# Optimization experiments

Measured on AMD Instinct MI355X. Metric: run time of the kernel, lower is better.

## Reference

```python
import jax, jax.numpy as jnp
import numpy as np

N_EMBD = 2048
N_HEAD = 32
N_GROUPS = 8
HEAD_DIM = N_EMBD // N_HEAD
Q_PER_KV = N_HEAD // N_GROUPS
QKV_DIM = (Q_PER_KV + 2) * N_GROUPS * HEAD_DIM


def apply_rope(x, cos, sin):
    # x: [B, nH, T, hd]; cos/sin: [T, rot//2]
    B, nH, T, hd = x.shape
    rot = min(sin.shape[1] * 2, hd)
    half = rot // 2
    x_rot, x_pass = x[..., :rot], x[..., rot:]
    c = cos[:T, :half][None, None]  # [1,1,T,half]
    s = sin[:T, :half][None, None]
    x1, x2 = x_rot[..., :half], x_rot[..., half:]
    x1_ = x1 * c - x2 * s
    x2_ = x2 * c + x1 * s
    return jnp.concatenate([x1_, x2_, x_pass], axis=-1)


def setup_inputs() -> dict:
    key = jax.random.key(0)
    k1, k2, k3, k4, k5 = jax.random.split(key, 5)
    B, T = 2, 2048
    x = jax.random.normal(k1, (B, T, N_EMBD), dtype=jnp.float32)
    cos = jax.random.uniform(k2, (T, HEAD_DIM // 2), dtype=jnp.float32)
    sin = jax.random.uniform(k3, (T, HEAD_DIM // 2), dtype=jnp.float32)
    attn_w = jax.random.normal(k4, (QKV_DIM, N_EMBD), dtype=jnp.float32) * (1.0 / np.sqrt(N_EMBD))
    proj_w = jax.random.normal(k5, (N_EMBD, N_EMBD), dtype=jnp.float32) * (1.0 / np.sqrt(N_EMBD))
    return {"x": x, "cos": cos, "sin": sin, "attn_w": attn_w, "proj_w": proj_w}


def reference(x, cos, sin, attn_w, proj_w):
    B, T, E = x.shape
    qkv = jnp.einsum('bte,fe->btf', x, attn_w)  # [B,T,QKV_DIM]
    qkv = qkv.reshape(B, T, N_GROUPS, Q_PER_KV + 2, HEAD_DIM)
    q = qkv[:, :, :, :Q_PER_KV].reshape(B, T, N_HEAD, HEAD_DIM)
    k = qkv[:, :, :, Q_PER_KV]      # [B,T,G,hd]
    v = qkv[:, :, :, Q_PER_KV + 1]  # [B,T,G,hd]
    # [B, heads, T, hd] layout; GQA repeat_interleave of K/V to full head count
    q = q.transpose(0, 2, 1, 3)
    k = jnp.repeat(k.transpose(0, 2, 1, 3), Q_PER_KV, axis=1)
    v = jnp.repeat(v.transpose(0, 2, 1, 3), Q_PER_KV, axis=1)
    q = apply_rope(q, cos, sin)
    k = apply_rope(k, cos, sin)
    scale = 1.0 / np.sqrt(HEAD_DIM)
    att = jax.nn.softmax(jnp.einsum('bhqd,bhkd->bhqk', q, k) * scale, axis=-1)
    out = jnp.einsum('bhqk,bhkd->bhqd', att, v)  # [B,nH,T,hd]
    out = out.transpose(0, 2, 1, 3).reshape(B, T, N_HEAD * HEAD_DIM)
    return jnp.einsum('bte,fe->btf', out, proj_w)
```

## Files before the change

### kernel.cpp

```cpp
#include <hip/hip_runtime.h>

typedef unsigned short u16;
typedef unsigned int u32;
typedef __bf16 bf16x8 __attribute__((ext_vector_type(8)));
typedef float f32x4 __attribute__((ext_vector_type(4)));
typedef float f32x16 __attribute__((ext_vector_type(16)));
typedef unsigned int u32x4 __attribute__((ext_vector_type(4)));

__device__ __forceinline__ u16 f2bf(float f) {
    u32 u = __builtin_bit_cast(u32, f);
    u32 r = u + 0x7FFFu + ((u >> 16) & 1u);
    return (u16)(r >> 16);
}
__device__ __forceinline__ u32 pack_bf16(float v0, float v1) {
    u32 a = __builtin_bit_cast(u32, v0) + 0x8000u;
    u32 b = __builtin_bit_cast(u32, v1) + 0x8000u;
    return __builtin_amdgcn_perm(b, a, 0x07060302u);
}
__device__ __forceinline__ u32 cvtpk(float lo, float hi) {
    u32 r;
    asm("v_cvt_pk_bf16_f32 %0, %1, %2" : "=v"(r) : "v"(lo), "v"(hi));
    return r;
}
__device__ __forceinline__ void plswap(u32& a, u32& b) {
    asm("v_permlane32_swap_b32 %0, %1" : "+v"(a), "+v"(b));
}
__device__ __forceinline__ void gload16(const u16* g, u16* l) {
    __builtin_amdgcn_global_load_lds(
        (const __attribute__((address_space(1))) u32*)g,
        (__attribute__((address_space(3))) u32*)l, 16, 0, 0);
}

#define QSCALE 0.18033688011111793f

__global__ __launch_bounds__(256) void cvt_kernel(const float* __restrict__ in,
                                                  u16* __restrict__ out, int n4) {
    int i = blockIdx.x * 256 + threadIdx.x;
    if (i >= n4) return;
    float4 f = reinterpret_cast<const float4*>(in)[i];
    u32 lo = (u32)f2bf(f.x) | ((u32)f2bf(f.y) << 16);
    u32 hi = (u32)f2bf(f.z) | ((u32)f2bf(f.w) << 16);
    reinterpret_cast<uint2*>(out)[i] = make_uint2(lo, hi);
}

__global__ __launch_bounds__(256) void gemm_qkv(const u16* __restrict__ A,
                                                const u16* __restrict__ Bw,
                                                const float* __restrict__ cosb,
                                                const float* __restrict__ sinb,
                                                u16* __restrict__ Qo,
                                                u16* __restrict__ Ko,
                                                u16* __restrict__ Vt) {
    __shared__ __align__(16) u16 As[2 * 128 * 32];
    __shared__ __align__(16) u16 Bs[2 * 128 * 32];
    const int tid = threadIdx.x;
    const int wave = tid >> 6, lane = tid & 63, quad = lane >> 4, l15 = lane & 15;
    const int wm = wave >> 1, wn = wave & 1;
    const int m0 = blockIdx.x * 128, n0 = blockIdx.y * 128;
    const int K = 2048;
    const int lrow = lane >> 2, lcol = (lane & 3) * 8;
    f32x4 acc[4][4];
#pragma unroll
    for (int a = 0; a < 4; a++)
#pragma unroll
        for (int b = 0; b < 4; b++) acc[a][b] = (f32x4){0.f, 0.f, 0.f, 0.f};
    for (int kk = 0; kk < K; kk += 64) {
        __syncthreads();
#pragma unroll
        for (int p = 0; p < 2; p++)
#pragma unroll
            for (int c = 0; c < 2; c++) {
                const int rA = wave * 32 + c * 16;
                gload16(A  + (size_t)(m0 + rA + lrow) * K + kk + p * 32 + lcol,
                        &As[p * 4096 + rA * 32]);
                gload16(Bw + (size_t)(n0 + rA + lrow) * K + kk + p * 32 + lcol,
                        &Bs[p * 4096 + rA * 32]);
            }
        __syncthreads();
#pragma unroll
        for (int p = 0; p < 2; p++) {
            bf16x8 af[4], bfr[4];
#pragma unroll
            for (int t = 0; t < 4; t++) {
                af[t]  = *reinterpret_cast<const bf16x8*>(
                    &As[p * 4096 + (wm * 64 + t * 16 + l15) * 32 + quad * 8]);
                bfr[t] = *reinterpret_cast<const bf16x8*>(
                    &Bs[p * 4096 + (wn * 64 + t * 16 + l15) * 32 + quad * 8]);
            }
#pragma unroll
            for (int tm = 0; tm < 4; tm++)
#pragma unroll
                for (int tn = 0; tn < 4; tn++)
                    acc[tm][tn] = __builtin_amdgcn_mfma_f32_16x16x32_bf16(af[tm], bfr[tn], acc[tm][tn], 0, 0, 0);
        }
    }
    const int slot_base = n0 + wn * 64;
    const int G = slot_base / 384;
    const int slot = (slot_base % 384) / 64;
    const int bb = m0 >> 11;
    const int tb0 = (m0 & 2047) + wm * 64 + quad * 4;
    if (slot == 5) {
        u16* vbase = Vt + ((size_t)(bb * 8 + G) * 64) * 2048;
#pragma unroll
        for (int tm = 0; tm < 4; tm++) {
            const int trow = tb0 + tm * 16;
#pragma unroll
            for (int tn = 0; tn < 4; tn++) {
                const int d = tn * 16 + l15;
                uint2 pk;
                pk.x = pack_bf16(acc[tm][tn][0], acc[tm][tn][1]);
                pk.y = pack_bf16(acc[tm][tn][2], acc[tm][tn][3]);
                *reinterpret_cast<uint2*>(vbase + (size_t)d * 2048 + trow) = pk;
            }
        }
    } else {
        const float sc = (slot < 4) ? QSCALE : 1.0f;
        u16* obase = (slot < 4)
            ? Qo + ((size_t)(bb * 32 + G * 4 + slot) * 2048) * 64
            : Ko + ((size_t)(bb * 8 + G) * 2048) * 64;
#pragma unroll
        for (int tm = 0; tm < 4; tm++) {
#pragma unroll
            for (int i = 0; i < 4; i++) {
                const int t = tb0 + tm * 16 + i;
#pragma unroll
                for (int tn = 0; tn < 2; tn++) {
                    const int dh = tn * 16 + l15;
                    float c = cosb[t * 32 + dh], s = sinb[t * 32 + dh];
                    float x1 = acc[tm][tn][i], x2 = acc[tm][tn + 2][i];
                    obase[(size_t)t * 64 + dh]      = f2bf((x1 * c - x2 * s) * sc);
                    obase[(size_t)t * 64 + dh + 32] = f2bf((x2 * c + x1 * s) * sc);
                }
            }
        }
    }
}

__global__ __launch_bounds__(256) void gemm_bt(const u16* __restrict__ A,
                                               const u16* __restrict__ Bw,
                                               float* __restrict__ Cf,
                                               int M, int N, int K) {
    __shared__ __align__(16) u16 As[2 * 128 * 32];
    __shared__ __align__(16) u16 Bs[2 * 128 * 32];
    const int tid = threadIdx.x;
    const int wave = tid >> 6, lane = tid & 63, quad = lane >> 4, l15 = lane & 15;
    const int wm = wave >> 1, wn = wave & 1;
    const int m0 = blockIdx.x * 128, n0 = blockIdx.y * 128;
    const int lrow = lane >> 2, lcol = (lane & 3) * 8;
    f32x4 acc[4][4];
#pragma unroll
    for (int a = 0; a < 4; a++)
#pragma unroll
        for (int b = 0; b < 4; b++) acc[a][b] = (f32x4){0.f, 0.f, 0.f, 0.f};
    for (int kk = 0; kk < K; kk += 64) {
        __syncthreads();
#pragma unroll
        for (int p = 0; p < 2; p++)
#pragma unroll
            for (int c = 0; c < 2; c++) {
                const int rA = wave * 32 + c * 16;
                gload16(A  + (size_t)(m0 + rA + lrow) * K + kk + p * 32 + lcol,
                        &As[p * 4096 + rA * 32]);
                gload16(Bw + (size_t)(n0 + rA + lrow) * K + kk + p * 32 + lcol,
                        &Bs[p * 4096 + rA * 32]);
            }
        __syncthreads();
#pragma unroll
        for (int p = 0; p < 2; p++) {
            bf16x8 af[4], bfr[4];
#pragma unroll
            for (int t = 0; t < 4; t++) {
                af[t]  = *reinterpret_cast<const bf16x8*>(
                    &As[p * 4096 + (wm * 64 + t * 16 + l15) * 32 + quad * 8]);
                bfr[t] = *reinterpret_cast<const bf16x8*>(
                    &Bs[p * 4096 + (wn * 64 + t * 16 + l15) * 32 + quad * 8]);
            }
#pragma unroll
            for (int tm = 0; tm < 4; tm++)
#pragma unroll
                for (int tn = 0; tn < 4; tn++)
                    acc[tm][tn] = __builtin_amdgcn_mfma_f32_16x16x32_bf16(af[tm], bfr[tn], acc[tm][tn], 0, 0, 0);
        }
    }
#pragma unroll
    for (int tm = 0; tm < 4; tm++) {
        const int r0 = m0 + wm * 64 + tm * 16 + quad * 4;
#pragma unroll
        for (int tn = 0; tn < 4; tn++) {
            const int c = n0 + wn * 64 + tn * 16 + l15;
#pragma unroll
            for (int i = 0; i < 4; i++) Cf[(size_t)(r0 + i) * N + c] = acc[tm][tn][i];
        }
    }
}

__global__ __launch_bounds__(256, 4) void attn(const u16* __restrict__ Q,
                                               const u16* __restrict__ Kg,
                                               const u16* __restrict__ Vt,
                                               u16* __restrict__ O) {
    __shared__ __align__(16) u16 Ks[2 * 64 * 64];
    __shared__ __align__(16) u16 Vts[2 * 64 * 64];
    const int tid = threadIdx.x, w = tid >> 6, lane = tid & 63;
    const int half = lane >> 5, l31 = lane & 31;
    const int rsub = lane >> 3;
    const int csub = (lane & 7) ^ rsub;
    const int swz = (l31 & 7) << 3;
    const int q0 = blockIdx.x * 128;
    const int h = blockIdx.y, b = blockIdx.z, g = h >> 2;
    const u16* qb = Q + (((size_t)(b * 32 + h)) * 2048 + q0) * 64;
    const u16* kb = Kg + ((size_t)(b * 8 + g)) * 2048 * 64;
    const u16* vb = Vt + ((size_t)(b * 8 + g)) * 64 * 2048;

#pragma unroll
    for (int i = 0; i < 4; i++) {
        const int r = w * 32 + i * 8;
        gload16(qb + (size_t)(r + rsub) * 64 + csub * 8, Ks + r * 64);
    }
    __syncthreads();
    bf16x8 qf[4];
#pragma unroll
    for (int ks = 0; ks < 4; ks++)
        qf[ks] = *reinterpret_cast<const bf16x8*>(
            &Ks[(w * 32 + l31) * 64 + ((ks * 16 + half * 8) ^ swz)]);
    __syncthreads();

    f32x16 Oa[2];
#pragma unroll
    for (int t = 0; t < 2; t++)
#pragma unroll
        for (int i = 0; i < 16; i++) Oa[t][i] = 0.f;
    float lsum = 0.f;

    auto stage_kv = [&](int kk, int bsel) {
        u16* kd = Ks + bsel * 4096;
        u16* vd = Vts + bsel * 4096;
        const u16* kg = kb + (size_t)kk * 64;
        const u16* vg = vb + kk;
#pragma unroll
        for (int i = 0; i < 2; i++) {
            const int r = w * 16 + i * 8;
            gload16(kg + (size_t)(r + rsub) * 64 + csub * 8, kd + r * 64);
            gload16(vg + (size_t)(r + rsub) * 2048 + csub * 8, vd + r * 64);
        }
    };

    stage_kv(0, 0);
    __syncthreads();

    for (int t = 0; t < 32; t++) {
        if (t < 31) stage_kv((t + 1) * 64, (t + 1) & 1);
        const u16* Kb = Ks + (t & 1) * 4096;
        const u16* Vb = Vts + (t & 1) * 4096;

        float ps = 0.f;
        u32 pw[4][4];
#pragma unroll
        for (int kt = 0; kt < 2; kt++) {
            f32x16 S;
#pragma unroll
            for (int i = 0; i < 16; i++) S[i] = 0.f;
            __builtin_amdgcn_s_setprio(1);
#pragma unroll
            for (int ks = 0; ks < 4; ks++) {
                bf16x8 kf = *reinterpret_cast<const bf16x8*>(
                    &Kb[(kt * 32 + l31) * 64 + ((ks * 16 + half * 8) ^ swz)]);
                S = __builtin_amdgcn_mfma_f32_32x32x16_bf16(kf, qf[ks], S, 0, 0, 0);
            }
            __builtin_amdgcn_s_setprio(0);
            float pe[16];
#pragma unroll
            for (int r = 0; r < 16; r++) pe[r] = __builtin_amdgcn_exp2f(S[r]);
#pragma unroll
            for (int r = 0; r < 4; r++)
                ps += (pe[r * 4 + 0] + pe[r * 4 + 1]) + (pe[r * 4 + 2] + pe[r * 4 + 3]);
#pragma unroll
            for (int j = 0; j < 2; j++) {
                u32 X0 = cvtpk(pe[j * 8 + 0], pe[j * 8 + 1]);
                u32 Y0 = cvtpk(pe[j * 8 + 4], pe[j * 8 + 5]);
                u32 X1 = cvtpk(pe[j * 8 + 2], pe[j * 8 + 3]);
                u32 Y1 = cvtpk(pe[j * 8 + 6], pe[j * 8 + 7]);
                plswap(X0, Y0);
                plswap(X1, Y1);
                const int ks2 = kt * 2 + j;
                pw[ks2][0] = X0; pw[ks2][1] = X1; pw[ks2][2] = Y0; pw[ks2][3] = Y1;
            }
        }
        lsum += ps;
        __builtin_amdgcn_s_setprio(1);
#pragma unroll
        for (int ks2 = 0; ks2 < 4; ks2++) {
            u32x4 pv = (u32x4){pw[ks2][0], pw[ks2][1], pw[ks2][2], pw[ks2][3]};
            bf16x8 pf = __builtin_bit_cast(bf16x8, pv);
#pragma unroll
            for (int dt = 0; dt < 2; dt++) {
                bf16x8 vf = *reinterpret_cast<const bf16x8*>(
                    &Vb[(dt * 32 + l31) * 64 + ((ks2 * 16 + half * 8) ^ swz)]);
                Oa[dt] = __builtin_amdgcn_mfma_f32_32x32x16_bf16(vf, pf, Oa[dt], 0, 0, 0);
            }
        }
        __builtin_amdgcn_s_setprio(0);
        __syncthreads();
    }
    float lt = lsum + __shfl_xor(lsum, 32);
    float linv = 1.f / lt;
    const int t = q0 + w * 32 + l31;
    u16* orow = O + ((size_t)(b * 2048 + t)) * 2048 + h * 64;
#pragma unroll
    for (int dt = 0; dt < 2; dt++)
#pragma unroll
        for (int gr = 0; gr < 4; gr++) {
            uint2 pk;
            pk.x = pack_bf16(Oa[dt][gr * 4 + 0] * linv, Oa[dt][gr * 4 + 1] * linv);
            pk.y = pack_bf16(Oa[dt][gr * 4 + 2] * linv, Oa[dt][gr * 4 + 3] * linv);
            *reinterpret_cast<uint2*>(orow + dt * 32 + 8 * gr + 4 * half) = pk;
        }
}

extern "C" void kernel_launch(void* const* d_in, const int* in_sizes, int n_in,
                              void* d_out, int out_size, void* d_ws, size_t ws_size,
                              hipStream_t stream) {
    const float* x      = (const float*)d_in[0];
    const float* cosb   = (const float*)d_in[1];
    const float* sinb   = (const float*)d_in[2];
    const float* attn_w = (const float*)d_in[3];
    const float* proj_w = (const float*)d_in[4];
    float* out = (float*)d_out;

    u16* xb  = (u16*)d_ws;
    u16* w1b = xb  + (size_t)4096 * 2048;
    u16* w2b = w1b + (size_t)3072 * 2048;
    u16* qo  = w2b + (size_t)2048 * 2048;
    u16* ko  = qo  + (size_t)2 * 32 * 2048 * 64;
    u16* vt  = ko  + (size_t)2 * 8 * 2048 * 64;
    u16* ao  = xb;

    cvt_kernel<<<8192, 256, 0, stream>>>(x, xb, 4096 * 2048 / 4);
    cvt_kernel<<<6144, 256, 0, stream>>>(attn_w, w1b, 3072 * 2048 / 4);
    cvt_kernel<<<4096, 256, 0, stream>>>(proj_w, w2b, 2048 * 2048 / 4);
    gemm_qkv<<<dim3(32, 24), 256, 0, stream>>>(xb, w1b, cosb, sinb, qo, ko, vt);
    attn<<<dim3(16, 32, 2), 256, 0, stream>>>(qo, ko, vt, ao);
    gemm_bt<<<dim3(32, 16), 256, 0, stream>>>(ao, w2b, out, 4096, 2048, 2048);
}
```

Baseline: 330.2 us.

## Enlarge QKV GEMM tiles to 256x256 with swizzled LDS double-buffering; merge conversion kernels

Rewrites the QKV projection GEMM to use 256x256 block tiles with 8 waves, a 64-wide K step and XOR-swizzled LDS layout. It double-buffers LDS so the next tile's global loads overlap the current MFMAs, and raises wave priority around the matrix ops. It also merges the three fp32-to-bf16 conversion launches into one kernel. The larger tile cuts global traffic per FLOP, but the grid shrinks to 192 blocks on a 256-CU part and LDS use rises to 128 KB per block, which could hurt occupancy.

```diff
diff --git a/kernel.cpp b/kernel.cpp
--- a/kernel.cpp
+++ b/kernel.cpp
@@ -33,82 +33,122 @@
 
 #define QSCALE 0.18033688011111793f
 
-__global__ __launch_bounds__(256) void cvt_kernel(const float* __restrict__ in,
-                                                  u16* __restrict__ out, int n4) {
+__global__ __launch_bounds__(256) void cvt3_kernel(const float* __restrict__ a, u16* __restrict__ ao,
+                                                   const float* __restrict__ b, u16* __restrict__ bo,
+                                                   const float* __restrict__ c, u16* __restrict__ co) {
     int i = blockIdx.x * 256 + threadIdx.x;
-    if (i >= n4) return;
-    float4 f = reinterpret_cast<const float4*>(in)[i];
+    const float* src; u16* dst; int idx;
+    if (i < 2097152)       { src = a; dst = ao; idx = i; }
+    else if (i < 3670016)  { src = b; dst = bo; idx = i - 2097152; }
+    else                   { src = c; dst = co; idx = i - 3670016; }
+    float4 f = reinterpret_cast<const float4*>(src)[idx];
     u32 lo = (u32)f2bf(f.x) | ((u32)f2bf(f.y) << 16);
     u32 hi = (u32)f2bf(f.z) | ((u32)f2bf(f.w) << 16);
-    reinterpret_cast<uint2*>(out)[i] = make_uint2(lo, hi);
-}
-
-__global__ __launch_bounds__(256) void gemm_qkv(const u16* __restrict__ A,
-                                                const u16* __restrict__ Bw,
-                                                const float* __restrict__ cosb,
-                                                const float* __restrict__ sinb,
-                                                u16* __restrict__ Qo,
-                                                u16* __restrict__ Ko,
-                                                u16* __restrict__ Vt) {
-    __shared__ __align__(16) u16 As[2 * 128 * 32];
-    __shared__ __align__(16) u16 Bs[2 * 128 * 32];
+    reinterpret_cast<uint2*>(dst)[idx] = make_uint2(lo, hi);
+}
+
+__global__ __launch_bounds__(512, 2) void gemm_qkv(const u16* __restrict__ A,
+                                                   const u16* __restrict__ Bw,
+                                                   const float* __restrict__ cosb,
+                                                   const float* __restrict__ sinb,
+                                                   u16* __restrict__ Qo,
+                                                   u16* __restrict__ Ko,
+                                                   u16* __restrict__ Vt) {
+    __shared__ __align__(16) u16 As[2 * 2 * 128 * 64];
+    __shared__ __align__(16) u16 Bs[2 * 2 * 128 * 64];
     const int tid = threadIdx.x;
-    const int wave = tid >> 6, lane = tid & 63, quad = lane >> 4, l15 = lane & 15;
-    const int wm = wave >> 1, wn = wave & 1;
-    const int m0 = blockIdx.x * 128, n0 = blockIdx.y * 128;
+    const int w = tid >> 6, lane = tid & 63;
+    const int quad = lane >> 4, l15 = lane & 15;
+    const int wr = w >> 2, wc = w & 3;
+    const int m0 = blockIdx.x * 256, n0 = blockIdx.y * 256;
     const int K = 2048;
-    const int lrow = lane >> 2, lcol = (lane & 3) * 8;
-    f32x4 acc[4][4];
-#pragma unroll
-    for (int a = 0; a < 4; a++)
+    const int rsub = lane >> 3;
+    const int csrc = (lane & 7) ^ rsub;
+    const int sx = (l15 & 7) << 3;
+    const int c0 = (quad * 8) ^ sx;
+    const int c1 = (32 + quad * 8) ^ sx;
+
+    f32x4 acc[8][4];
+#pragma unroll
+    for (int a = 0; a < 8; a++)
 #pragma unroll
         for (int b = 0; b < 4; b++) acc[a][b] = (f32x4){0.f, 0.f, 0.f, 0.f};
-    for (int kk = 0; kk < K; kk += 64) {
-        __syncthreads();
-#pragma unroll
-        for (int p = 0; p < 2; p++)
-#pragma unroll
-            for (int c = 0; c < 2; c++) {
-                const int rA = wave * 32 + c * 16;
-                gload16(A  + (size_t)(m0 + rA + lrow) * K + kk + p * 32 + lcol,
-                        &As[p * 4096 + rA * 32]);
-                gload16(Bw + (size_t)(n0 + rA + lrow) * K + kk + p * 32 + lcol,
-                        &Bs[p * 4096 + rA * 32]);
-            }
-        __syncthreads();
-#pragma unroll
-        for (int p = 0; p < 2; p++) {
-            bf16x8 af[4], bfr[4];
-#pragma unroll
-            for (int t = 0; t < 4; t++) {
-                af[t]  = *reinterpret_cast<const bf16x8*>(
-                    &As[p * 4096 + (wm * 64 + t * 16 + l15) * 32 + quad * 8]);
-                bfr[t] = *reinterpret_cast<const bf16x8*>(
-                    &Bs[p * 4096 + (wn * 64 + t * 16 + l15) * 32 + quad * 8]);
-            }
-#pragma unroll
-            for (int tm = 0; tm < 4; tm++)
-#pragma unroll
-                for (int tn = 0; tn < 4; tn++)
-                    acc[tm][tn] = __builtin_amdgcn_mfma_f32_16x16x32_bf16(af[tm], bfr[tn], acc[tm][tn], 0, 0, 0);
-        }
-    }
-    const int slot_base = n0 + wn * 64;
-    const int G = slot_base / 384;
-    const int slot = (slot_base % 384) / 64;
+
+    auto stage = [&](const u16* g, int row0, int kk, u16* lds) {
+#pragma unroll
+        for (int i = 0; i < 2; i++)
+            gload16(g + (size_t)(row0 + (i * 8 + w) * 8 + rsub) * K + kk + csrc * 8,
+                    lds + (i * 8 + w) * 512);
+    };
+
+    stage(A,  m0,       0, &As[0]);
+    stage(A,  m0 + 128, 0, &As[8192]);
+    stage(Bw, n0,       0, &Bs[0]);
+    stage(Bw, n0 + 128, 0, &Bs[8192]);
+    asm volatile("s_waitcnt vmcnt(0)" ::: "memory");
+    __builtin_amdgcn_s_barrier();
+
+    for (int j = 0; j < 32; ++j) {
+        const int cur = j & 1;
+        const u16* Ab = &As[cur * 16384 + wr * 8192];
+        const u16* Bb = &Bs[cur * 16384 + (wc >> 1) * 8192 + (wc & 1) * 4096];
+        u16* Asn = &As[(cur ^ 1) * 16384];
+        u16* Bsn = &Bs[(cur ^ 1) * 16384];
+        const int kk2 = (j + 1) * 64;
+        bf16x8 af[4][2];
+#pragma unroll
+        for (int q = 0; q < 4; ++q) {
+            const int qm = q >> 1, qn = q & 1;
+            if (qn == 0) {
+#pragma unroll
+                for (int fm = 0; fm < 4; fm++) {
+                    af[fm][0] = *reinterpret_cast<const bf16x8*>(&Ab[(qm * 64 + fm * 16 + l15) * 64 + c0]);
+                    af[fm][1] = *reinterpret_cast<const bf16x8*>(&Ab[(qm * 64 + fm * 16 + l15) * 64 + c1]);
+                }
+            }
+            bf16x8 bfv[2][2];
+#pragma unroll
+            for (int fn = 0; fn < 2; fn++) {
+                bfv[fn][0] = *reinterpret_cast<const bf16x8*>(&Bb[(qn * 32 + fn * 16 + l15) * 64 + c0]);
+                bfv[fn][1] = *reinterpret_cast<const bf16x8*>(&Bb[(qn * 32 + fn * 16 + l15) * 64 + c1]);
+            }
+            if (j < 31) {
+                if (q == 0)      { stage(A,  m0,       kk2, Asn); stage(A,  m0 + 128, kk2, Asn + 8192); }
+                else if (q == 1) { stage(Bw, n0,       kk2, Bsn); stage(Bw, n0 + 128, kk2, Bsn + 8192); }
+            }
+            __builtin_amdgcn_s_barrier();
+            __builtin_amdgcn_s_setprio(1);
+#pragma unroll
+            for (int fm = 0; fm < 4; fm++)
+#pragma unroll
+                for (int fn = 0; fn < 2; fn++) {
+                    acc[qm * 4 + fm][qn * 2 + fn] = __builtin_amdgcn_mfma_f32_16x16x32_bf16(
+                        af[fm][0], bfv[fn][0], acc[qm * 4 + fm][qn * 2 + fn], 0, 0, 0);
+                    acc[qm * 4 + fm][qn * 2 + fn] = __builtin_amdgcn_mfma_f32_16x16x32_bf16(
+                        af[fm][1], bfv[fn][1], acc[qm * 4 + fm][qn * 2 + fn], 0, 0, 0);
+                }
+            __builtin_amdgcn_s_setprio(0);
+            if (q == 3 && j < 31) asm volatile("s_waitcnt vmcnt(0)" ::: "memory");
+            __builtin_amdgcn_s_barrier();
+        }
+    }
+
+    const int nw0 = n0 + wc * 64;
+    const int G = nw0 / 384;
+    const int slot = (nw0 % 384) / 64;
     const int bb = m0 >> 11;
-    const int tb0 = (m0 & 2047) + wm * 64 + quad * 4;
+    const int tb0 = (m0 & 2047) + wr * 128 + quad * 4;
     if (slot == 5) {
         u16* vbase = Vt + ((size_t)(bb * 8 + G) * 64) * 2048;
 #pragma unroll
-        for (int tm = 0; tm < 4; tm++) {
-            const int trow = tb0 + tm * 16;
-#pragma unroll
-            for (int tn = 0; tn < 4; tn++) {
-                const int d = tn * 16 + l15;
+        for (int fm = 0; fm < 8; fm++) {
+            const int trow = tb0 + fm * 16;
+#pragma unroll
+            for (int fn = 0; fn < 4; fn++) {
+                const int d = fn * 16 + l15;
                 uint2 pk;
-                pk.x = pack_bf16(acc[tm][tn][0], acc[tm][tn][1]);
-                pk.y = pack_bf16(acc[tm][tn][2], acc[tm][tn][3]);
+                pk.x = pack_bf16(acc[fm][fn][0], acc[fm][fn][1]);
+                pk.y = pack_bf16(acc[fm][fn][2], acc[fm][fn][3]);
                 *reinterpret_cast<uint2*>(vbase + (size_t)d * 2048 + trow) = pk;
             }
         }
@@ -118,15 +158,15 @@
             ? Qo + ((size_t)(bb * 32 + G * 4 + slot) * 2048) * 64
             : Ko + ((size_t)(bb * 8 + G) * 2048) * 64;
 #pragma unroll
-        for (int tm = 0; tm < 4; tm++) {
+        for (int fm = 0; fm < 8; fm++) {
 #pragma unroll
             for (int i = 0; i < 4; i++) {
-                const int t = tb0 + tm * 16 + i;
-#pragma unroll
-                for (int tn = 0; tn < 2; tn++) {
-                    const int dh = tn * 16 + l15;
+                const int t = tb0 + fm * 16 + i;
+#pragma unroll
+                for (int fn = 0; fn < 2; fn++) {
+                    const int dh = fn * 16 + l15;
                     float c = cosb[t * 32 + dh], s = sinb[t * 32 + dh];
-                    float x1 = acc[tm][tn][i], x2 = acc[tm][tn + 2][i];
+                    float x1 = acc[fm][fn][i], x2 = acc[fm][fn + 2][i];
                     obase[(size_t)t * 64 + dh]      = f2bf((x1 * c - x2 * s) * sc);
                     obase[(size_t)t * 64 + dh + 32] = f2bf((x2 * c + x1 * s) * sc);
                 }
@@ -333,10 +373,8 @@
     u16* vt  = ko  + (size_t)2 * 8 * 2048 * 64;
     u16* ao  = xb;
 
-    cvt_kernel<<<8192, 256, 0, stream>>>(x, xb, 4096 * 2048 / 4);
-    cvt_kernel<<<6144, 256, 0, stream>>>(attn_w, w1b, 3072 * 2048 / 4);
-    cvt_kernel<<<4096, 256, 0, stream>>>(proj_w, w2b, 2048 * 2048 / 4);
-    gemm_qkv<<<dim3(32, 24), 256, 0, stream>>>(xb, w1b, cosb, sinb, qo, ko, vt);
+    cvt3_kernel<<<18432, 256, 0, stream>>>(x, xb, attn_w, w1b, proj_w, w2b);
+    gemm_qkv<<<dim3(16, 12), 512, 0, stream>>>(xb, w1b, cosb, sinb, qo, ko, vt);
     attn<<<dim3(16, 32, 2), 256, 0, stream>>>(qo, ko, vt, ao);
     gemm_bt<<<dim3(32, 16), 256, 0, stream>>>(ao, w2b, out, 4096, 2048, 2048);
 }
```

Result: faster. 311.5 us (-5.7%).
